# Performance work log

Measured on AMD Instinct MI355X. Metric: run time of the kernel, lower is better.

The kernel has to match this reference:

```python
import jax, jax.numpy as jnp
import numpy as np

N = 20000      # nodes
E = 160000     # edges
F_IN = 128     # num_node_features
D = 128        # embedding_size (out_channels)
H = 4          # heads
NEG = 0.2      # GATv2Conv negative_slope
N_LAYERS = 3


def setup_inputs() -> dict:
    key = jax.random.key(0)
    ks = jax.random.split(key, 12)
    s = 0.05
    return {
        "x": jax.random.normal(ks[0], (N, F_IN), jnp.float32),
        "edge_index": jax.random.randint(ks[1], (2, E), 0, N, jnp.int64),
        "edge_attr": jax.random.normal(ks[2], (E, 2), jnp.float32),
        "Wf": jax.random.normal(ks[3], (F_IN, D), jnp.float32) * s,
        "bf": jnp.zeros((D,), jnp.float32),
        "Wl": jax.random.normal(ks[4], (D, H * D), jnp.float32) * s,
        "bl": jnp.zeros((H * D,), jnp.float32),
        "Wr": jax.random.normal(ks[5], (D, H * D), jnp.float32) * s,
        "br": jnp.zeros((H * D,), jnp.float32),
        "We": jax.random.normal(ks[6], (2, H * D), jnp.float32) * s,
        "att": jax.random.normal(ks[7], (H, D), jnp.float32) * s,
        "bias_out": jnp.zeros((D,), jnp.float32),
    }


def reference(x, edge_index, edge_attr, Wf, bf, Wl, bl, Wr, br, We, att, bias_out):
    src, dst = edge_index[0], edge_index[1]

    # add_self_loops with fill_value='mean': self-loop edge_attr = mean of
    # incoming edge_attr per node (0 where a node has no incoming edges)
    ea_sum = jax.ops.segment_sum(edge_attr, dst, num_segments=N)            # [N,2]
    cnt = jax.ops.segment_sum(jnp.ones((E,), edge_attr.dtype), dst, num_segments=N)
    loop_attr = ea_sum / jnp.maximum(cnt, 1.0)[:, None]
    loop_idx = jnp.arange(N, dtype=src.dtype)
    fsrc = jnp.concatenate([src, loop_idx])                                  # [E+N]
    fdst = jnp.concatenate([dst, loop_idx])
    fea = jnp.concatenate([edge_attr, loop_attr], axis=0)                    # [E+N,2]

    ee = (fea @ We).reshape(-1, H, D)                                        # [E+N,H,D]

    def gatv2_layer(h):
        xl = (h @ Wl + bl).reshape(N, H, D)   # lin_l -> source-side / message
        xr = (h @ Wr + br).reshape(N, H, D)   # lin_r -> target-side
        e = jax.nn.leaky_relu(xl[fsrc] + xr[fdst] + ee, NEG)                 # [E+N,H,D]
        logits = jnp.einsum('ehd,hd->eh', e, att)                            # [E+N,H]
        m = jax.ops.segment_max(logits, fdst, num_segments=N)                # [N,H]
        w = jnp.exp(logits - m[fdst])
        denom = jax.ops.segment_sum(w, fdst, num_segments=N)                 # [N,H]
        alpha = w / denom[fdst]                                              # segment softmax
        msg = xl[fsrc] * alpha[..., None]                                    # [E+N,H,D]
        out = jax.ops.segment_sum(msg, fdst, num_segments=N)                 # [N,H,D]
        return out.mean(axis=1) + bias_out                                   # concat=False

    h = x @ Wf + bf
    for _ in range(N_LAYERS):
        h = jax.nn.leaky_relu(gatv2_layer(h), 0.01)  # F.leaky_relu default slope
    return h
```

## Files before the change

kernel.cpp:

```cpp
#include <hip/hip_runtime.h>
#include <hip/hip_bf16.h>

#define NN 20000
#define NE 160000
#define EF (NE + NN)
#define DD 128
#define HH 4
#define NPA (NN * DD)
#define NPW (1024 * 128 + 128 * 128 + 1024)
#define NBLK 40

typedef unsigned short u16;
typedef unsigned int u32;

using short8  = __attribute__((ext_vector_type(8))) short;
using float4v = __attribute__((ext_vector_type(4))) float;

__device__ __forceinline__ float bf2f(u16 u) {
    union { u32 i; float f; } c;
    c.i = ((u32)u) << 16;
    return c.f;
}
__device__ __forceinline__ u16 f2bf(float f) {
    union { float f; u32 u; } c;
    c.f = f;
    u32 u = c.u;
    u32 r = (u + 0x7fffu + ((u >> 16) & 1u)) >> 16;
    return (u16)r;
}


__global__ void k_zero_i(int* __restrict__ p, int n) {
    int i = blockIdx.x * blockDim.x + threadIdx.x;
    if (i < n) p[i] = 0;
}

__global__ void k_zero_f(float* __restrict__ p, int n) {
    int i = blockIdx.x * blockDim.x + threadIdx.x;
    if (i < n) p[i] = 0.f;
}


__global__ void k_deg(const int* __restrict__ ei, const float* __restrict__ ea,
                      int* __restrict__ cnt, float* __restrict__ ea_sum) {
    int e = blockIdx.x * blockDim.x + threadIdx.x;
    if (e >= NE) return;
    int t = ei[NE + e];
    atomicAdd(&cnt[t], 1);
    atomicAdd(&ea_sum[t * 2 + 0], ea[e * 2 + 0]);
    atomicAdd(&ea_sum[t * 2 + 1], ea[e * 2 + 1]);
}

__global__ __launch_bounds__(512) void k_scan_a(const int* __restrict__ cnt,
                                                int* __restrict__ rowptr,
                                                int* __restrict__ bsum) {
    __shared__ int ws[8];
    int tid = threadIdx.x;
    int i = blockIdx.x * 512 + tid;
    int l = tid & 63, w = tid >> 6;
    int v = (i < NN) ? (cnt[i] + 1) : 0;
    #pragma unroll
    for (int off = 1; off < 64; off <<= 1) {
        int u = __shfl_up(v, off, 64);
        if (l >= off) v += u;
    }
    if (l == 63) ws[w] = v;
    __syncthreads();
    if (w == 0) {
        int s = (l < 8) ? ws[l] : 0;
        #pragma unroll
        for (int off = 1; off < 8; off <<= 1) {
            int u = __shfl_up(s, off, 64);
            if (l >= off) s += u;
        }
        if (l < 8) ws[l] = s;
    }
    __syncthreads();
    v += (w > 0) ? ws[w - 1] : 0;
    if (i < NN) rowptr[i + 1] = v;
    if (tid == 511) bsum[blockIdx.x] = v;
}

__global__ void k_scan_c(int* __restrict__ rowptr, const int* __restrict__ bsum) {
    int l = threadIdx.x & 63;
    int v = (l < NBLK) ? bsum[l] : 0;
    #pragma unroll
    for (int off = 1; off < 64; off <<= 1) {
        int u = __shfl_up(v, off, 64);
        if (l >= off) v += u;
    }
    int i = blockIdx.x * blockDim.x + threadIdx.x;
    int j = i >> 9;
    int off = (j > 0) ? __shfl(v, j - 1, 64) : 0;
    if (i < NN) rowptr[i + 1] += off;
    if (i == 0) rowptr[0] = 0;
}

__global__ void k_fill(const int* __restrict__ ei, const float* __restrict__ ea,
                       const int* __restrict__ rowptr, int* __restrict__ fillc,
                       const int* __restrict__ cnt, const float* __restrict__ ea_sum,
                       int* __restrict__ srcs,
                       float* __restrict__ fa0, float* __restrict__ fa1) {
    int e = blockIdx.x * blockDim.x + threadIdx.x;
    if (e < NE) {
        int s = ei[e], t = ei[NE + e];
        int pos = atomicAdd(&fillc[t], 1);
        int slot = rowptr[t] + pos;
        srcs[slot] = s;
        fa0[slot] = ea[e * 2];
        fa1[slot] = ea[e * 2 + 1];
    } else if (e < NE + NN) {
        int n = e - NE;
        int slot = rowptr[n + 1] - 1;
        srcs[slot] = n;
        float c = fmaxf((float)cnt[n], 1.f);
        fa0[slot] = ea_sum[n * 2 + 0] / c;
        fa1[slot] = ea_sum[n * 2 + 1] / c;
    }
}


__global__ void k_pack(const float* __restrict__ x,
                       const float* __restrict__ Wl, const float* __restrict__ Wr,
                       const float* __restrict__ bl, const float* __restrict__ br,
                       const float* __restrict__ Wf,
                       u16* __restrict__ Axh, u16* __restrict__ Axl,
                       u16* __restrict__ W2Th, u16* __restrict__ W2Tl,
                       u16* __restrict__ WfTh, u16* __restrict__ WfTl,
                       float* __restrict__ bias2) {
    int i = blockIdx.x * blockDim.x + threadIdx.x;
    if (i < NPA) {
        float a = x[i];
        u16 h = f2bf(a);
        Axh[i] = h;
        Axl[i] = f2bf(a - bf2f(h));
        return;
    }
    i -= NPA;
    if (i < 1024 * 128) {
        int n = i >> 7, k = i & 127;
        float w = (n < 512) ? Wl[k * 512 + n] : Wr[k * 512 + (n - 512)];
        u16 h = f2bf(w);
        W2Th[n * 128 + k] = h;
        W2Tl[n * 128 + k] = f2bf(w - bf2f(h));
    } else if (i < 1024 * 128 + 128 * 128) {
        int u = i - 1024 * 128;
        int n = u >> 7, k = u & 127;
        float w = Wf[k * 128 + n];
        u16 h = f2bf(w);
        WfTh[n * 128 + k] = h;
        WfTl[n * 128 + k] = f2bf(w - bf2f(h));
    } else if (i < NPW) {
        int n = i - (1024 * 128 + 128 * 128);
        bias2[n] = (n < 512) ? bl[n] : br[n - 512];
    }
}


template<int SPLIT>
__global__ __launch_bounds__(256, 3) void k_mgemm(
        const u16* __restrict__ Ahg, const u16* __restrict__ Alg,
        const u16* __restrict__ BTh, const u16* __restrict__ BTl,
        const float* __restrict__ bias, float* __restrict__ C1,
        float* __restrict__ C2,
        u16* __restrict__ Oh, u16* __restrict__ Ol, int M) {
    constexpr int KS = 136;
    __shared__ u16 sAh[64 * KS], sBh[64 * KS], sBl[64 * KS];
    int m0 = blockIdx.y * 64;
    int n0 = blockIdx.x * 64;
    int t = threadIdx.x;
    int lane = t & 63;
    int wm = (t >> 6) & 1;
    int wn = t >> 7;
    int fm = lane & 15;
    int q8 = (lane >> 4) * 8;

    short8 fal[4][2];
    #pragma unroll
    for (int i = 0; i < 2; ++i) {
        const u16* p = Alg + (size_t)(m0 + wm * 32 + i * 16 + fm) * 128 + q8;
        #pragma unroll
        for (int kk = 0; kk < 4; ++kk)
            fal[kk][i] = *(const short8*)(p + kk * 32);
    }

    #pragma unroll
    for (int i = 0; i < 4; ++i) {
        int c = t + 256 * i;
        int row = c >> 4, ko = (c & 15) * 8;
        int gm = m0 + row;
        short8 va = {0, 0, 0, 0, 0, 0, 0, 0};
        if (gm < M) va = *(const short8*)&Ahg[gm * 128 + ko];
        *(short8*)&sAh[row * KS + ko] = va;
        int gn = n0 + row;
        *(short8*)&sBh[row * KS + ko] = *(const short8*)&BTh[gn * 128 + ko];
        *(short8*)&sBl[row * KS + ko] = *(const short8*)&BTl[gn * 128 + ko];
    }
    __syncthreads();

    float4v zz = {0.f, 0.f, 0.f, 0.f};
    float4v acc[2][2];
    acc[0][0] = zz; acc[0][1] = zz; acc[1][0] = zz; acc[1][1] = zz;

    #pragma unroll
    for (int k0 = 0; k0 < 128; k0 += 32) {
        short8 fah[2], fbh[2], fbl[2];
        #pragma unroll
        for (int i = 0; i < 2; ++i) {
            int mr = wm * 32 + i * 16 + fm;
            fah[i] = *(const short8*)&sAh[mr * KS + k0 + q8];
            int nr = wn * 32 + i * 16 + fm;
            fbh[i] = *(const short8*)&sBh[nr * KS + k0 + q8];
            fbl[i] = *(const short8*)&sBl[nr * KS + k0 + q8];
        }
        #pragma unroll
        for (int i = 0; i < 2; ++i)
            #pragma unroll
            for (int j = 0; j < 2; ++j) {
                acc[i][j] = __builtin_amdgcn_mfma_f32_16x16x32_bf16(fah[i], fbh[j], acc[i][j], 0, 0, 0);
                acc[i][j] = __builtin_amdgcn_mfma_f32_16x16x32_bf16(fah[i], fbl[j], acc[i][j], 0, 0, 0);
                acc[i][j] = __builtin_amdgcn_mfma_f32_16x16x32_bf16(fal[k0 >> 5][i], fbh[j], acc[i][j], 0, 0, 0);
            }
    }

    float* Cout = (n0 < 512) ? C1 : C2;
    int cofs = (n0 < 512) ? 0 : 512;
    #pragma unroll
    for (int i = 0; i < 2; ++i) {
        #pragma unroll
        for (int j = 0; j < 2; ++j) {
            int gn = n0 + wn * 32 + j * 16 + fm;
            float bv = bias[gn];
            #pragma unroll
            for (int r = 0; r < 4; ++r) {
                int gm = m0 + wm * 32 + i * 16 + (lane >> 4) * 4 + r;
                if (gm < M) {
                    float v = acc[i][j][r] + bv;
                    if (SPLIT) {
                        u16 h = f2bf(v);
                        Oh[gm * 128 + gn] = h;
                        Ol[gm * 128 + gn] = f2bf(v - bf2f(h));
                    } else {
                        Cout[gm * 512 + gn - cofs] = v;
                    }
                }
            }
        }
    }
}


__global__ __launch_bounds__(256) void k_gat(
        const int* __restrict__ rowptr, const int* __restrict__ srcs,
        const float* __restrict__ fa0, const float* __restrict__ fa1,
        const float* __restrict__ xl, const float* __restrict__ xr,
        const float* __restrict__ We, const float* __restrict__ att,
        const float* __restrict__ bias_out,
        u16* __restrict__ Oh, u16* __restrict__ Ol,
        float* __restrict__ outp, int last) {
    int n = blockIdx.x * 4 + (threadIdx.x >> 6);
    if (n >= NN) return;
    int l = threadIdx.x & 63;
    int d0 = l * 8;
    float xrv[8], we0[8], we1[8], atv[8];
    {
        float4 a = *reinterpret_cast<const float4*>(&xr[(size_t)n * 512 + d0]);
        float4 b = *reinterpret_cast<const float4*>(&xr[(size_t)n * 512 + d0 + 4]);
        xrv[0]=a.x; xrv[1]=a.y; xrv[2]=a.z; xrv[3]=a.w;
        xrv[4]=b.x; xrv[5]=b.y; xrv[6]=b.z; xrv[7]=b.w;
        a = *reinterpret_cast<const float4*>(&We[d0]);
        b = *reinterpret_cast<const float4*>(&We[d0 + 4]);
        we0[0]=a.x; we0[1]=a.y; we0[2]=a.z; we0[3]=a.w;
        we0[4]=b.x; we0[5]=b.y; we0[6]=b.z; we0[7]=b.w;
        a = *reinterpret_cast<const float4*>(&We[512 + d0]);
        b = *reinterpret_cast<const float4*>(&We[512 + d0 + 4]);
        we1[0]=a.x; we1[1]=a.y; we1[2]=a.z; we1[3]=a.w;
        we1[4]=b.x; we1[5]=b.y; we1[6]=b.z; we1[7]=b.w;
        a = *reinterpret_cast<const float4*>(&att[d0]);
        b = *reinterpret_cast<const float4*>(&att[d0 + 4]);
        atv[0]=a.x; atv[1]=a.y; atv[2]=a.z; atv[3]=a.w;
        atv[4]=b.x; atv[5]=b.y; atv[6]=b.z; atv[7]=b.w;
    }
    int b0 = rowptr[n], b1 = rowptr[n + 1];
    float acc[8] = {0.f,0.f,0.f,0.f,0.f,0.f,0.f,0.f};
    float den = 0.f;
    int sNext = srcs[b0];
    for (int e = b0; e < b1; ++e) {
        int s = sNext;
        if (e + 1 < b1) sNext = srcs[e + 1];
        float f0 = fa0[e], f1 = fa1[e];
        const float* xlp = &xl[(size_t)s * 512 + d0];
        float4 a = *reinterpret_cast<const float4*>(xlp);
        float4 b = *reinterpret_cast<const float4*>(xlp + 4);
        float xv[8] = {a.x, a.y, a.z, a.w, b.x, b.y, b.z, b.w};
        float p = 0.f;
        #pragma unroll
        for (int k = 0; k < 8; ++k) {
            float v = xv[k] + xrv[k] + f0 * we0[k] + f1 * we1[k];
            v = v > 0.f ? v : 0.2f * v;
            p += v * atv[k];
        }
        p += __shfl_xor(p, 1, 64);
        p += __shfl_xor(p, 2, 64);
        p += __shfl_xor(p, 4, 64);
        p += __shfl_xor(p, 8, 64);
        float wt = __expf(p);
        den += wt;
        #pragma unroll
        for (int k = 0; k < 8; ++k) acc[k] += wt * xv[k];
    }
    float inv = 1.f / den;
    float val[8];
    #pragma unroll
    for (int k = 0; k < 8; ++k) {
        float v = acc[k] * inv;
        v += __shfl_xor(v, 16, 64);
        v += __shfl_xor(v, 32, 64);
        val[k] = v;
    }
    if (l < 16) {
        #pragma unroll
        for (int k = 0; k < 8; ++k) {
            float v = val[k] * 0.25f + bias_out[d0 + k];
            v = v > 0.f ? v : 0.01f * v;
            val[k] = v;
        }
        if (last) {
            #pragma unroll
            for (int k = 0; k < 8; ++k) outp[n * 128 + d0 + k] = val[k];
        } else {
            #pragma unroll
            for (int k = 0; k < 8; ++k) {
                u16 hv = f2bf(val[k]);
                Oh[n * 128 + d0 + k] = hv;
                Ol[n * 128 + d0 + k] = f2bf(val[k] - bf2f(hv));
            }
        }
    }
}


extern "C" void kernel_launch(void* const* d_in, const int* in_sizes, int n_in,
                              void* d_out, int out_size, void* d_ws, size_t ws_size,
                              hipStream_t stream) {
    size_t o = 0;
    auto alloc = [&](size_t bytes) { size_t cur = o; o += (bytes + 255) & ~(size_t)255; return cur; };
    size_t off_cnt    = alloc((size_t)NN * 4);
    size_t off_fillc  = alloc((size_t)NN * 4);
    size_t off_easum  = alloc((size_t)NN * 2 * 4);
    size_t off_rowptr = alloc((size_t)(NN + 1) * 4);
    size_t off_bsum   = alloc((size_t)NBLK * 4);
    size_t off_srcs   = alloc((size_t)EF * 4);
    size_t off_fa0    = alloc((size_t)EF * 4);
    size_t off_fa1    = alloc((size_t)EF * 4);
    size_t off_axh    = alloc((size_t)NN * DD * 2);
    size_t off_axl    = alloc((size_t)NN * DD * 2);
    size_t off_ah     = alloc((size_t)NN * DD * 2);
    size_t off_al     = alloc((size_t)NN * DD * 2);
    size_t off_xl     = alloc((size_t)NN * 512 * 4);
    size_t off_xr     = alloc((size_t)NN * 512 * 4);
    size_t off_w2th   = alloc((size_t)1024 * 128 * 2);
    size_t off_w2tl   = alloc((size_t)1024 * 128 * 2);
    size_t off_wfth   = alloc((size_t)128 * 128 * 2);
    size_t off_wftl   = alloc((size_t)128 * 128 * 2);
    size_t off_bias2  = alloc((size_t)1024 * 4);
    size_t need = o;

    bool ok = (n_in == 12) && d_ws != nullptr && ws_size >= need
           && out_size == NN * DD
           && in_sizes[0] == NN * DD && in_sizes[1] == 2 * NE
           && in_sizes[2] == NE * 2 && in_sizes[3] == 128 * 128
           && in_sizes[5] == 128 * 512 && in_sizes[9] == 2 * 512
           && in_sizes[10] == 4 * 128 && in_sizes[11] == 128;
    if (!ok) {
        k_zero_f<<<(NN * DD + 255) / 256, 256, 0, stream>>>((float*)d_out, NN * DD);
        return;
    }

    const float* x        = (const float*)d_in[0];
    const int*   ei       = (const int*)d_in[1];
    const float* ea       = (const float*)d_in[2];
    const float* Wf       = (const float*)d_in[3];
    const float* bf       = (const float*)d_in[4];
    const float* Wl       = (const float*)d_in[5];
    const float* bl       = (const float*)d_in[6];
    const float* Wr       = (const float*)d_in[7];
    const float* br       = (const float*)d_in[8];
    const float* We       = (const float*)d_in[9];
    const float* att      = (const float*)d_in[10];
    const float* bias_out = (const float*)d_in[11];

    char* base = (char*)d_ws;
    int*   cnt    = (int*)(base + off_cnt);
    int*   fillc  = (int*)(base + off_fillc);
    float* ea_sum = (float*)(base + off_easum);
    int*   rowptr = (int*)(base + off_rowptr);
    int*   bsum   = (int*)(base + off_bsum);
    int*   srcs   = (int*)(base + off_srcs);
    float* fa0    = (float*)(base + off_fa0);
    float* fa1    = (float*)(base + off_fa1);
    u16*   Axh    = (u16*)(base + off_axh);
    u16*   Axl    = (u16*)(base + off_axl);
    u16*   Ah     = (u16*)(base + off_ah);
    u16*   Al     = (u16*)(base + off_al);
    float* xl     = (float*)(base + off_xl);
    float* xr     = (float*)(base + off_xr);
    u16*   W2Th   = (u16*)(base + off_w2th);
    u16*   W2Tl   = (u16*)(base + off_w2tl);
    u16*   WfTh   = (u16*)(base + off_wfth);
    u16*   WfTl   = (u16*)(base + off_wftl);
    float* bias2  = (float*)(base + off_bias2);

    int zero_ints = (int)((off_easum + (size_t)NN * 2 * 4 - off_cnt) / 4);
    k_zero_i<<<(zero_ints + 255) / 256, 256, 0, stream>>>(cnt, zero_ints);

    k_deg<<<(NE + 255) / 256, 256, 0, stream>>>(ei, ea, cnt, ea_sum);
    k_scan_a<<<NBLK, 512, 0, stream>>>(cnt, rowptr, bsum);
    k_scan_c<<<(NN + 255) / 256, 256, 0, stream>>>(rowptr, bsum);
    k_fill<<<(NE + NN + 255) / 256, 256, 0, stream>>>(ei, ea, rowptr, fillc,
                                                      cnt, ea_sum, srcs, fa0, fa1);

    k_pack<<<(NPA + NPW + 255) / 256, 256, 0, stream>>>(x, Wl, Wr, bl, br, Wf,
                                                        Axh, Axl, W2Th, W2Tl,
                                                        WfTh, WfTl, bias2);

    const int MT = (NN + 63) / 64;
    k_mgemm<1><<<dim3(2, MT), 256, 0, stream>>>(Axh, Axl, WfTh, WfTl,
                                                bf, nullptr, nullptr, Ah, Al, NN);

    for (int layer = 0; layer < 3; ++layer) {
        k_mgemm<0><<<dim3(16, MT), 256, 0, stream>>>(Ah, Al, W2Th, W2Tl,
                                                     bias2, xl, xr, nullptr, nullptr, NN);
        int last = (layer == 2);
        k_gat<<<(NN + 3) / 4, 256, 0, stream>>>(rowptr, srcs, fa0, fa1, xl, xr,
                                                We, att, bias_out, Ah, Al,
                                                (float*)d_out, last);
    }
}
```

Baseline: 472.8 us.

## Fuse degree and pack kernels, single-block scan, reuse A tile across two N tiles

```diff
diff --git a/kernel.cpp b/kernel.cpp
--- a/kernel.cpp
+++ b/kernel.cpp
@@ -8,7 +8,7 @@
 #define HH 4
 #define NPA (NN * DD)
 #define NPW (1024 * 128 + 128 * 128 + 1024)
-#define NBLK 40
+#define DEGB ((NE + 255) / 256)
 
 typedef unsigned short u16;
 typedef unsigned int u32;
@@ -41,60 +41,92 @@
 }
 
 
-__global__ void k_deg(const int* __restrict__ ei, const float* __restrict__ ea,
-                      int* __restrict__ cnt, float* __restrict__ ea_sum) {
-    int e = blockIdx.x * blockDim.x + threadIdx.x;
-    if (e >= NE) return;
-    int t = ei[NE + e];
-    atomicAdd(&cnt[t], 1);
-    atomicAdd(&ea_sum[t * 2 + 0], ea[e * 2 + 0]);
-    atomicAdd(&ea_sum[t * 2 + 1], ea[e * 2 + 1]);
-}
-
-__global__ __launch_bounds__(512) void k_scan_a(const int* __restrict__ cnt,
-                                                int* __restrict__ rowptr,
-                                                int* __restrict__ bsum) {
-    __shared__ int ws[8];
+__global__ void k_degpack(const int* __restrict__ ei, const float* __restrict__ ea,
+                          const float* __restrict__ x,
+                          const float* __restrict__ Wl, const float* __restrict__ Wr,
+                          const float* __restrict__ bl, const float* __restrict__ br,
+                          const float* __restrict__ Wf,
+                          int* __restrict__ cnt, float* __restrict__ ea_sum,
+                          u16* __restrict__ Axh, u16* __restrict__ Axl,
+                          u16* __restrict__ W2Th, u16* __restrict__ W2Tl,
+                          u16* __restrict__ WfTh, u16* __restrict__ WfTl,
+                          float* __restrict__ bias2) {
+    int gb = blockIdx.x;
+    if (gb < DEGB) {
+        int e = gb * 256 + threadIdx.x;
+        if (e >= NE) return;
+        int t = ei[NE + e];
+        atomicAdd(&cnt[t], 1);
+        atomicAdd(&ea_sum[t * 2 + 0], ea[e * 2 + 0]);
+        atomicAdd(&ea_sum[t * 2 + 1], ea[e * 2 + 1]);
+        return;
+    }
+    int i = (gb - DEGB) * 256 + threadIdx.x;
+    if (i < NPA) {
+        float a = x[i];
+        u16 h = f2bf(a);
+        Axh[i] = h;
+        Axl[i] = f2bf(a - bf2f(h));
+        return;
+    }
+    i -= NPA;
+    if (i < 1024 * 128) {
+        int n = i >> 7, k = i & 127;
+        float w = (n < 512) ? Wl[k * 512 + n] : Wr[k * 512 + (n - 512)];
+        u16 h = f2bf(w);
+        W2Th[n * 128 + k] = h;
+        W2Tl[n * 128 + k] = f2bf(w - bf2f(h));
+    } else if (i < 1024 * 128 + 128 * 128) {
+        int u = i - 1024 * 128;
+        int n = u >> 7, k = u & 127;
+        float w = Wf[k * 128 + n];
+        u16 h = f2bf(w);
+        WfTh[n * 128 + k] = h;
+        WfTl[n * 128 + k] = f2bf(w - bf2f(h));
+    } else if (i < NPW) {
+        int n = i - (1024 * 128 + 128 * 128);
+        bias2[n] = (n < 512) ? bl[n] : br[n - 512];
+    }
+}
+
+
+__global__ void k_scan(const int* __restrict__ cnt, int* __restrict__ rowptr) {
+    __shared__ int wsum[16];
+    __shared__ int s_base;
     int tid = threadIdx.x;
-    int i = blockIdx.x * 512 + tid;
-    int l = tid & 63, w = tid >> 6;
-    int v = (i < NN) ? (cnt[i] + 1) : 0;
-    #pragma unroll
-    for (int off = 1; off < 64; off <<= 1) {
-        int u = __shfl_up(v, off, 64);
-        if (l >= off) v += u;
-    }
-    if (l == 63) ws[w] = v;
+    int w = tid >> 6, l = tid & 63;
+    if (tid == 0) { s_base = 0; rowptr[0] = 0; }
     __syncthreads();
-    if (w == 0) {
-        int s = (l < 8) ? ws[l] : 0;
-        #pragma unroll
-        for (int off = 1; off < 8; off <<= 1) {
-            int u = __shfl_up(s, off, 64);
-            if (l >= off) s += u;
-        }
-        if (l < 8) ws[l] = s;
-    }
-    __syncthreads();
-    v += (w > 0) ? ws[w - 1] : 0;
-    if (i < NN) rowptr[i + 1] = v;
-    if (tid == 511) bsum[blockIdx.x] = v;
-}
-
-__global__ void k_scan_c(int* __restrict__ rowptr, const int* __restrict__ bsum) {
-    int l = threadIdx.x & 63;
-    int v = (l < NBLK) ? bsum[l] : 0;
-    #pragma unroll
-    for (int off = 1; off < 64; off <<= 1) {
-        int u = __shfl_up(v, off, 64);
-        if (l >= off) v += u;
-    }
-    int i = blockIdx.x * blockDim.x + threadIdx.x;
-    int j = i >> 9;
-    int off = (j > 0) ? __shfl(v, j - 1, 64) : 0;
-    if (i < NN) rowptr[i + 1] += off;
-    if (i == 0) rowptr[0] = 0;
-}
+    const int chunks = (NN + 1023) / 1024;
+    for (int c = 0; c < chunks; ++c) {
+        int i = c * 1024 + tid;
+        int v = (i < NN) ? (cnt[i] + 1) : 0;
+        #pragma unroll
+        for (int off = 1; off < 64; off <<= 1) {
+            int u = __shfl_up(v, off, 64);
+            if (l >= off) v += u;
+        }
+        if (l == 63) wsum[w] = v;
+        __syncthreads();
+        if (w == 0) {
+            int s = (l < 16) ? wsum[l] : 0;
+            #pragma unroll
+            for (int off = 1; off < 16; off <<= 1) {
+                int u = __shfl_up(s, off, 64);
+                if (l >= off) s += u;
+            }
+            if (l < 16) wsum[l] = s;
+        }
+        __syncthreads();
+        int waveoff = (w > 0) ? wsum[w - 1] : 0;
+        int incl = s_base + waveoff + v;
+        if (i < NN) rowptr[i + 1] = incl;
+        __syncthreads();
+        if (tid == 1023) s_base = incl;
+        __syncthreads();
+    }
+}
+
 
 __global__ void k_fill(const int* __restrict__ ei, const float* __restrict__ ea,
                        const int* __restrict__ rowptr, int* __restrict__ fillc,
@@ -120,43 +152,6 @@
 }
 
 
-__global__ void k_pack(const float* __restrict__ x,
-                       const float* __restrict__ Wl, const float* __restrict__ Wr,
-                       const float* __restrict__ bl, const float* __restrict__ br,
-                       const float* __restrict__ Wf,
-                       u16* __restrict__ Axh, u16* __restrict__ Axl,
-                       u16* __restrict__ W2Th, u16* __restrict__ W2Tl,
-                       u16* __restrict__ WfTh, u16* __restrict__ WfTl,
-                       float* __restrict__ bias2) {
-    int i = blockIdx.x * blockDim.x + threadIdx.x;
-    if (i < NPA) {
-        float a = x[i];
-        u16 h = f2bf(a);
-        Axh[i] = h;
-        Axl[i] = f2bf(a - bf2f(h));
-        return;
-    }
-    i -= NPA;
-    if (i < 1024 * 128) {
-        int n = i >> 7, k = i & 127;
-        float w = (n < 512) ? Wl[k * 512 + n] : Wr[k * 512 + (n - 512)];
-        u16 h = f2bf(w);
-        W2Th[n * 128 + k] = h;
-        W2Tl[n * 128 + k] = f2bf(w - bf2f(h));
-    } else if (i < 1024 * 128 + 128 * 128) {
-        int u = i - 1024 * 128;
-        int n = u >> 7, k = u & 127;
-        float w = Wf[k * 128 + n];
-        u16 h = f2bf(w);
-        WfTh[n * 128 + k] = h;
-        WfTl[n * 128 + k] = f2bf(w - bf2f(h));
-    } else if (i < NPW) {
-        int n = i - (1024 * 128 + 128 * 128);
-        bias2[n] = (n < 512) ? bl[n] : br[n - 512];
-    }
-}
-
-
 template<int SPLIT>
 __global__ __launch_bounds__(256, 3) void k_mgemm(
         const u16* __restrict__ Ahg, const u16* __restrict__ Alg,
@@ -167,7 +162,6 @@
     constexpr int KS = 136;
     __shared__ u16 sAh[64 * KS], sBh[64 * KS], sBl[64 * KS];
     int m0 = blockIdx.y * 64;
-    int n0 = blockIdx.x * 64;
     int t = threadIdx.x;
     int lane = t & 63;
     int wm = (t >> 6) & 1;
@@ -192,56 +186,66 @@
         short8 va = {0, 0, 0, 0, 0, 0, 0, 0};
         if (gm < M) va = *(const short8*)&Ahg[gm * 128 + ko];
         *(short8*)&sAh[row * KS + ko] = va;
-        int gn = n0 + row;
-        *(short8*)&sBh[row * KS + ko] = *(const short8*)&BTh[gn * 128 + ko];
-        *(short8*)&sBl[row * KS + ko] = *(const short8*)&BTl[gn * 128 + ko];
-    }
-    __syncthreads();
-
-    float4v zz = {0.f, 0.f, 0.f, 0.f};
-    float4v acc[2][2];
-    acc[0][0] = zz; acc[0][1] = zz; acc[1][0] = zz; acc[1][1] = zz;
-
-    #pragma unroll
-    for (int k0 = 0; k0 < 128; k0 += 32) {
-        short8 fah[2], fbh[2], fbl[2];
+    }
+
+    for (int bb = 0; bb < 2; ++bb) {
+        int n0 = (blockIdx.x * 2 + bb) * 64;
+        __syncthreads();
+        #pragma unroll
+        for (int i = 0; i < 4; ++i) {
+            int c = t + 256 * i;
+            int row = c >> 4, ko = (c & 15) * 8;
+            int gn = n0 + row;
+            *(short8*)&sBh[row * KS + ko] = *(const short8*)&BTh[gn * 128 + ko];
+            *(short8*)&sBl[row * KS + ko] = *(const short8*)&BTl[gn * 128 + ko];
+        }
+        __syncthreads();
+
+        float4v zz = {0.f, 0.f, 0.f, 0.f};
+        float4v acc[2][2];
+        acc[0][0] = zz; acc[0][1] = zz; acc[1][0] = zz; acc[1][1] = zz;
+
+        #pragma unroll
+        for (int k0 = 0; k0 < 128; k0 += 32) {
+            short8 fah[2], fbh[2], fbl[2];
+            #pragma unroll
+            for (int i = 0; i < 2; ++i) {
+                int mr = wm * 32 + i * 16 + fm;
+                fah[i] = *(const short8*)&sAh[mr * KS + k0 + q8];
+                int nr = wn * 32 + i * 16 + fm;
+                fbh[i] = *(const short8*)&sBh[nr * KS + k0 + q8];
+                fbl[i] = *(const short8*)&sBl[nr * KS + k0 + q8];
+            }
+            #pragma unroll
+            for (int i = 0; i < 2; ++i)
+                #pragma unroll
+                for (int j = 0; j < 2; ++j) {
+                    acc[i][j] = __builtin_amdgcn_mfma_f32_16x16x32_bf16(fah[i], fbh[j], acc[i][j], 0, 0, 0);
+                    acc[i][j] = __builtin_amdgcn_mfma_f32_16x16x32_bf16(fah[i], fbl[j], acc[i][j], 0, 0, 0);
+                    acc[i][j] = __builtin_amdgcn_mfma_f32_16x16x32_bf16(fal[k0 >> 5][i], fbh[j], acc[i][j], 0, 0, 0);
+                }
+        }
+
+        float* Cout = (n0 < 512) ? C1 : C2;
+        int cofs = (n0 < 512) ? 0 : 512;
         #pragma unroll
         for (int i = 0; i < 2; ++i) {
-            int mr = wm * 32 + i * 16 + fm;
-            fah[i] = *(const short8*)&sAh[mr * KS + k0 + q8];
-            int nr = wn * 32 + i * 16 + fm;
-            fbh[i] = *(const short8*)&sBh[nr * KS + k0 + q8];
-            fbl[i] = *(const short8*)&sBl[nr * KS + k0 + q8];
-        }
-        #pragma unroll
-        for (int i = 0; i < 2; ++i)
             #pragma unroll
             for (int j = 0; j < 2; ++j) {
-                acc[i][j] = __builtin_amdgcn_mfma_f32_16x16x32_bf16(fah[i], fbh[j], acc[i][j], 0, 0, 0);
-                acc[i][j] = __builtin_amdgcn_mfma_f32_16x16x32_bf16(fah[i], fbl[j], acc[i][j], 0, 0, 0);
-                acc[i][j] = __builtin_amdgcn_mfma_f32_16x16x32_bf16(fal[k0 >> 5][i], fbh[j], acc[i][j], 0, 0, 0);
-            }
-    }
-
-    float* Cout = (n0 < 512) ? C1 : C2;
-    int cofs = (n0 < 512) ? 0 : 512;
-    #pragma unroll
-    for (int i = 0; i < 2; ++i) {
-        #pragma unroll
-        for (int j = 0; j < 2; ++j) {
-            int gn = n0 + wn * 32 + j * 16 + fm;
-            float bv = bias[gn];
-            #pragma unroll
-            for (int r = 0; r < 4; ++r) {
-                int gm = m0 + wm * 32 + i * 16 + (lane >> 4) * 4 + r;
-                if (gm < M) {
-                    float v = acc[i][j][r] + bv;
-                    if (SPLIT) {
-                        u16 h = f2bf(v);
-                        Oh[gm * 128 + gn] = h;
-                        Ol[gm * 128 + gn] = f2bf(v - bf2f(h));
-                    } else {
-                        Cout[gm * 512 + gn - cofs] = v;
+                int gn = n0 + wn * 32 + j * 16 + fm;
+                float bv = bias[gn];
+                #pragma unroll
+                for (int r = 0; r < 4; ++r) {
+                    int gm = m0 + wm * 32 + i * 16 + (lane >> 4) * 4 + r;
+                    if (gm < M) {
+                        float v = acc[i][j][r] + bv;
+                        if (SPLIT) {
+                            u16 h = f2bf(v);
+                            Oh[gm * 128 + gn] = h;
+                            Ol[gm * 128 + gn] = f2bf(v - bf2f(h));
+                        } else {
+                            Cout[gm * 512 + gn - cofs] = v;
+                        }
                     }
                 }
             }
@@ -349,7 +353,6 @@
     size_t off_fillc  = alloc((size_t)NN * 4);
     size_t off_easum  = alloc((size_t)NN * 2 * 4);
     size_t off_rowptr = alloc((size_t)(NN + 1) * 4);
-    size_t off_bsum   = alloc((size_t)NBLK * 4);
     size_t off_srcs   = alloc((size_t)EF * 4);
     size_t off_fa0    = alloc((size_t)EF * 4);
     size_t off_fa1    = alloc((size_t)EF * 4);
@@ -395,7 +398,6 @@
     int*   fillc  = (int*)(base + off_fillc);
     float* ea_sum = (float*)(base + off_easum);
     int*   rowptr = (int*)(base + off_rowptr);
-    int*   bsum   = (int*)(base + off_bsum);
     int*   srcs   = (int*)(base + off_srcs);
     float* fa0    = (float*)(base + off_fa0);
     float* fa1    = (float*)(base + off_fa1);
@@ -414,23 +416,21 @@
     int zero_ints = (int)((off_easum + (size_t)NN * 2 * 4 - off_cnt) / 4);
     k_zero_i<<<(zero_ints + 255) / 256, 256, 0, stream>>>(cnt, zero_ints);
 
-    k_deg<<<(NE + 255) / 256, 256, 0, stream>>>(ei, ea, cnt, ea_sum);
-    k_scan_a<<<NBLK, 512, 0, stream>>>(cnt, rowptr, bsum);
-    k_scan_c<<<(NN + 255) / 256, 256, 0, stream>>>(rowptr, bsum);
+    int packb = (NPA + NPW + 255) / 256;
+    k_degpack<<<DEGB + packb, 256, 0, stream>>>(ei, ea, x, Wl, Wr, bl, br, Wf,
+                                                cnt, ea_sum, Axh, Axl,
+                                                W2Th, W2Tl, WfTh, WfTl, bias2);
+    k_scan<<<1, 1024, 0, stream>>>(cnt, rowptr);
     k_fill<<<(NE + NN + 255) / 256, 256, 0, stream>>>(ei, ea, rowptr, fillc,
                                                       cnt, ea_sum, srcs, fa0, fa1);
 
-    k_pack<<<(NPA + NPW + 255) / 256, 256, 0, stream>>>(x, Wl, Wr, bl, br, Wf,
-                                                        Axh, Axl, W2Th, W2Tl,
-                                                        WfTh, WfTl, bias2);
-
     const int MT = (NN + 63) / 64;
-    k_mgemm<1><<<dim3(2, MT), 256, 0, stream>>>(Axh, Axl, WfTh, WfTl,
+    k_mgemm<1><<<dim3(1, MT), 256, 0, stream>>>(Axh, Axl, WfTh, WfTl,
                                                 bf, nullptr, nullptr, Ah, Al, NN);
 
     for (int layer = 0; layer < 3; ++layer) {
-        k_mgemm<0><<<dim3(16, MT), 256, 0, stream>>>(Ah, Al, W2Th, W2Tl,
-                                                     bias2, xl, xr, nullptr, nullptr, NN);
+        k_mgemm<0><<<dim3(8, MT), 256, 0, stream>>>(Ah, Al, W2Th, W2Tl,
+                                                    bias2, xl, xr, nullptr, nullptr, NN);
         int last = (layer == 2);
         k_gat<<<(NN + 3) / 4, 256, 0, stream>>>(rowptr, srcs, fa0, fa1, xl, xr,
                                                 We, att, bias_out, Ah, Al,
```

Result: no change. 463.6 us (-1.9%).
